# Kernel tuning notes

Measured on AMD Instinct MI355X. Metric: run time of the kernel, lower is better.

## Reference

```python
import jax, jax.numpy as jnp
import numpy as np

N_NODES = 100000


def gcn_conv(x, src, dst, W, b, n_nodes):
    # GCNConv: h = x @ W, then symmetric-normalized aggregation (self-loops already in src/dst)
    h = x @ W  # [N, out]
    ones = jnp.ones(src.shape[0], dtype=h.dtype)
    deg = jax.ops.segment_sum(ones, dst, num_segments=n_nodes)  # in-degree incl. self-loop
    dinv = jnp.where(deg > 0, jax.lax.rsqrt(deg), 0.0)
    norm = dinv[src] * dinv[dst]  # [E]
    msg = h[src] * norm[:, None]  # [E, out] gather
    out = jax.ops.segment_sum(msg, dst, num_segments=n_nodes)  # scatter-add
    return out + b


def setup_inputs() -> dict:
    key = jax.random.key(0)
    k1, k2, k3, k4 = jax.random.split(key, 4)
    n, f, h, c, e = N_NODES, 256, 128, 40, 1600000
    x = jax.random.normal(k1, (n, f), dtype=jnp.float32)
    edge_index = jax.random.randint(k2, (2, e), 0, n, dtype=jnp.int64)
    W1 = jax.random.normal(k3, (f, h), dtype=jnp.float32) * (1.0 / np.sqrt(f))
    b1 = jnp.zeros((h,), dtype=jnp.float32)
    W2 = jax.random.normal(k4, (h, c), dtype=jnp.float32) * (1.0 / np.sqrt(h))
    b2 = jnp.zeros((c,), dtype=jnp.float32)
    return {"x": x, "edge_index": edge_index, "W1": W1, "b1": b1, "W2": W2, "b2": b2}


def reference(x, edge_index, W1, b1, W2, b2):
    n = x.shape[0]
    loops = jnp.arange(n, dtype=edge_index.dtype)
    src = jnp.concatenate([edge_index[0], loops])
    dst = jnp.concatenate([edge_index[1], loops])
    h = jax.nn.relu(gcn_conv(x, src, dst, W1, b1, n))
    # dropout is identity in eval mode (self.training == False)
    logits = gcn_conv(h, src, dst, W2, b2, n)
    return jax.nn.log_softmax(logits, axis=1)
```

## Files before the change

### kernel.cpp

```cpp
#include <hip/hip_runtime.h>
#include <hip/hip_fp16.h>
#include <math.h>

#define FIN 256
#define HID 128
#define NCLS 40
#define ZPB 64
#define BKT_SHIFT 9
#define BKT_SZ 512
#define CHUNK 2048
#define CAP 12288

typedef __attribute__((ext_vector_type(8))) short short8_t;
typedef __attribute__((ext_vector_type(8))) _Float16 half8_t;
typedef __attribute__((ext_vector_type(4))) float f32x4;
typedef __attribute__((ext_vector_type(2))) float f32x2;

static __device__ __forceinline__ ushort f2bf(float f) {
    unsigned u = __float_as_uint(f);
    u += 0x7FFF + ((u >> 16) & 1);
    return (ushort)(u >> 16);
}

static __device__ __forceinline__ unsigned pack_ew(int s, float w) {
    return ((unsigned)s << 15) | (__float_as_uint(w) >> 17);
}


__global__ void k_prep(int* __restrict__ bcur, const float* __restrict__ W1,
                       ushort* __restrict__ Wt, const float* __restrict__ W2,
                       __half* __restrict__ W2t, int nbk) {
    int i = blockIdx.x * 256 + threadIdx.x;
    if (i <= nbk) bcur[i] = 0;
    if (i < FIN * HID) {
        int c = i >> 8, k = i & 255;
        Wt[i] = f2bf(W1[(size_t)k * HID + c]);
    }
    if (i < 48 * HID) {
        int c = i >> 7, k = i & 127;
        W2t[i] = __float2half((c < NCLS) ? W2[(size_t)k * NCLS + c] : 0.f);
    }
}


__global__ __launch_bounds__(256) void k_g1bkt(const float* __restrict__ X,
                                               const ushort* __restrict__ Wt,
                                               unsigned char* __restrict__ H8, int M,
                                               const int* __restrict__ src,
                                               const int* __restrict__ dst, int E,
                                               int* __restrict__ bcur,
                                               unsigned* __restrict__ ebkt,
                                               int nbk, int nbkb) {
    __shared__ uint4 wlds[128 * 32];
    int tid = threadIdx.x;

    if ((int)blockIdx.x < nbkb) {
        int* hist  = (int*)wlds;
        int* scanb = hist + 256;
        int* base  = scanb + 256;
        int* gbase = base + 256;
        unsigned* stage = (unsigned*)(gbase + 256);
        unsigned char* sbk = (unsigned char*)(stage + CHUNK);
        int e0 = blockIdx.x * CHUNK;
        int cntc = min(CHUNK, E - e0);
        hist[tid] = 0;
        __syncthreads();

        int s_[8], d_[8], bk_[8], rk_[8];
#pragma unroll
        for (int i = 0; i < 8; i++) {
            int j = tid + i * 256;
            if (j < cntc) {
                int s = src[e0 + j], d = dst[e0 + j];
                s_[i] = s; d_[i] = d;
                bk_[i] = d >> BKT_SHIFT;
                rk_[i] = atomicAdd(&hist[bk_[i]], 1);
            } else {
                bk_[i] = -1;
            }
        }
        __syncthreads();

        scanb[tid] = hist[tid];
        __syncthreads();
        for (int o = 1; o < 256; o <<= 1) {
            int u = (tid >= o) ? scanb[tid - o] : 0;
            __syncthreads();
            scanb[tid] += u;
            __syncthreads();
        }
        base[tid] = scanb[tid] - hist[tid];
        if (tid < nbk && hist[tid] > 0) gbase[tid] = atomicAdd(&bcur[tid], hist[tid]);
        __syncthreads();

#pragma unroll
        for (int i = 0; i < 8; i++) {
            if (bk_[i] >= 0) {
                int p = base[bk_[i]] + rk_[i];
                stage[p] = ((unsigned)s_[i] << 9) | ((unsigned)d_[i] & 511u);
                sbk[p] = (unsigned char)bk_[i];
            }
        }
        __syncthreads();

#pragma unroll
        for (int i = 0; i < 8; i++) {
            int j = tid + i * 256;
            if (j < cntc) {
                int bk = sbk[j];
                ebkt[(size_t)bk * CAP + gbase[bk] + (j - base[bk])] = stage[j];
            }
        }
        return;
    }

    int bid = blockIdx.x - nbkb;
    const uint4* wg = (const uint4*)Wt;
#pragma unroll
    for (int i = 0; i < 16; i++) {
        int e = tid + i * 256;
        int r = e >> 5, ch = e & 31;
        wlds[r * 32 + (ch ^ (r & 7))] = wg[e];
    }

    int wid = tid >> 6, lane = tid & 63;
    int q = lane & 15, kg = lane >> 4;
    int grow_in = bid * 64 + wid * 16 + q;
    int lrow = min(grow_in, M - 1);
    const float* xr = X + (size_t)lrow * FIN;

    float4 xf0[8], xf1[8];
#pragma unroll
    for (int kt = 0; kt < 8; kt++) {
        int k0 = kt * 32 + kg * 8;
        xf0[kt] = *(const float4*)(xr + k0);
        xf1[kt] = *(const float4*)(xr + k0 + 4);
    }
    __syncthreads();

    f32x4 acc[8];
#pragma unroll
    for (int c = 0; c < 8; c++) acc[c] = (f32x4){0.f, 0.f, 0.f, 0.f};

#pragma unroll
    for (int kt = 0; kt < 8; kt++) {
        unsigned r0, r1, r2, r3;
        asm("v_cvt_pk_bf16_f32 %0, %1, %2" : "=v"(r0) : "v"(xf0[kt].x), "v"(xf0[kt].y));
        asm("v_cvt_pk_bf16_f32 %0, %1, %2" : "=v"(r1) : "v"(xf0[kt].z), "v"(xf0[kt].w));
        asm("v_cvt_pk_bf16_f32 %0, %1, %2" : "=v"(r2) : "v"(xf1[kt].x), "v"(xf1[kt].y));
        asm("v_cvt_pk_bf16_f32 %0, %1, %2" : "=v"(r3) : "v"(xf1[kt].z), "v"(xf1[kt].w));
        union { uint4 u; short8_t s; } cv;
        cv.u = make_uint4(r0, r1, r2, r3);
        short8_t a = cv.s;
        int ch = kt * 4 + kg;
#pragma unroll
        for (int c = 0; c < 8; c++) {
            int col = c * 16 + q;
            short8_t b = *(const short8_t*)&wlds[col * 32 + (ch ^ (col & 7))];
            acc[c] = __builtin_amdgcn_mfma_f32_16x16x32_bf16(a, b, acc[c], 0, 0, 0);
        }
    }

    __syncthreads();
    float* st = (float*)wlds;
#pragma unroll
    for (int c = 0; c < 8; c++) {
        int col = c * 16 + q;
#pragma unroll
        for (int i = 0; i < 4; i++) {
            int lr = wid * 16 + kg * 4 + i;
            st[lr * 132 + col] = acc[c][i];
        }
    }
    __syncthreads();
    int orow = tid >> 2, seg = tid & 3;
    int grow = bid * 64 + orow;
    if (grow < M) {
        const float* sp = st + orow * 132 + seg * 32;
        unsigned u[8];
#pragma unroll
        for (int k = 0; k < 8; k++) {
            int p = 0;
            p = __builtin_amdgcn_cvt_pk_fp8_f32(sp[4 * k + 0], sp[4 * k + 1], p, false);
            p = __builtin_amdgcn_cvt_pk_fp8_f32(sp[4 * k + 2], sp[4 * k + 3], p, true);
            u[k] = (unsigned)p;
        }
        uint4* op = (uint4*)(H8 + (size_t)grow * HID + seg * 32);
        op[0] = make_uint4(u[0], u[1], u[2], u[3]);
        op[1] = make_uint4(u[4], u[5], u[6], u[7]);
    }
}


__global__ __launch_bounds__(512) void k_cnt(const unsigned* __restrict__ ebkt,
                                             int* __restrict__ bcur, int nbk,
                                             int* __restrict__ off, int* __restrict__ cnt,
                                             float* __restrict__ dinv, int n) {
    __shared__ int lcnt[BKT_SZ];
    __shared__ int lofs[BKT_SZ];
    __shared__ int lbase;
    int b = blockIdx.x, t = threadIdx.x;
    int n0 = b << BKT_SHIFT;
    lcnt[t] = 0;
    __syncthreads();
    int sz = bcur[b];
    const unsigned* ep = ebkt + (size_t)b * CAP;
    for (int e = t; e < sz; e += 512) atomicAdd(&lcnt[ep[e] & 511u], 1);
    __syncthreads();
    if (t == 0) lbase = atomicAdd(&bcur[nbk], sz);
    lofs[t] = lcnt[t];
    __syncthreads();
    for (int o = 1; o < 512; o <<= 1) {
        int u = (t >= o) ? lofs[t - o] : 0;
        __syncthreads();
        lofs[t] += u;
        __syncthreads();
    }
    int node = n0 + t;
    if (node < n) {
        int c = lcnt[t];
        off[node] = lbase + lofs[t] - c;
        cnt[node] = c;
        dinv[node] = rsqrtf((float)(c + 1));
    }
}


__global__ __launch_bounds__(512) void k_place(const unsigned* __restrict__ ebkt,
                                               const int* __restrict__ bcur,
                                               const int* __restrict__ off,
                                               const float* __restrict__ dinv,
                                               unsigned* __restrict__ eew, int n) {
    __shared__ int curx[BKT_SZ];
    __shared__ float ldin[BKT_SZ];
    int b = blockIdx.x, t = threadIdx.x;
    int n0 = b << BKT_SHIFT;
    int node = n0 + t;
    if (node < n) {
        curx[t] = off[node];
        ldin[t] = dinv[node];
    }
    __syncthreads();
    int sz = bcur[b];
    const unsigned* ep = ebkt + (size_t)b * CAP;
    for (int e = t; e < sz; e += 512) {
        unsigned ed = ep[e];
        int s = (int)(ed >> 9), dl = (int)(ed & 511u);
        float w = dinv[s] * ldin[dl];
        int pos = atomicAdd(&curx[dl], 1);
        eew[pos] = pack_ew(s, w);
    }
}


__global__ __launch_bounds__(256) void k_agg1(const unsigned char* __restrict__ H8,
                                              const unsigned* __restrict__ eew,
                                              const int* __restrict__ off,
                                              const int* __restrict__ cnt,
                                              const float* __restrict__ dinv,
                                              const float* __restrict__ b1,
                                              __half* __restrict__ H2, int n) {
    int tid = threadIdx.x;
    int node = blockIdx.x * 16 + (tid >> 4);
    int q = tid & 15;
    if (node >= n) return;
    float di = dinv[node];
    int start = off[node], ne = cnt[node];

    float acc[8];
    {
        uint2 v = *(const uint2*)(H8 + (size_t)node * HID + q * 8);
        float wv = di * di;
        f32x2 f;
        f = __builtin_amdgcn_cvt_pk_f32_fp8((int)v.x, false);
        acc[0] = f[0] * wv; acc[1] = f[1] * wv;
        f = __builtin_amdgcn_cvt_pk_f32_fp8((int)v.x, true);
        acc[2] = f[0] * wv; acc[3] = f[1] * wv;
        f = __builtin_amdgcn_cvt_pk_f32_fp8((int)v.y, false);
        acc[4] = f[0] * wv; acc[5] = f[1] * wv;
        f = __builtin_amdgcn_cvt_pk_f32_fp8((int)v.y, true);
        acc[6] = f[0] * wv; acc[7] = f[1] * wv;
    }

#pragma unroll 2
    for (int j = 0; j < ne; ++j) {
        unsigned u = eew[start + j];
        int s = (int)(u >> 15);
        float wv = __uint_as_float((u & 0x7FFFu) << 17);
        uint2 v = *(const uint2*)(H8 + (size_t)s * HID + q * 8);
        f32x2 f;
        f = __builtin_amdgcn_cvt_pk_f32_fp8((int)v.x, false);
        acc[0] = fmaf(f[0], wv, acc[0]); acc[1] = fmaf(f[1], wv, acc[1]);
        f = __builtin_amdgcn_cvt_pk_f32_fp8((int)v.x, true);
        acc[2] = fmaf(f[0], wv, acc[2]); acc[3] = fmaf(f[1], wv, acc[3]);
        f = __builtin_amdgcn_cvt_pk_f32_fp8((int)v.y, false);
        acc[4] = fmaf(f[0], wv, acc[4]); acc[5] = fmaf(f[1], wv, acc[5]);
        f = __builtin_amdgcn_cvt_pk_f32_fp8((int)v.y, true);
        acc[6] = fmaf(f[0], wv, acc[6]); acc[7] = fmaf(f[1], wv, acc[7]);
    }

    float r[8];
#pragma unroll
    for (int i = 0; i < 8; i++) r[i] = fmaxf(acc[i] + b1[q * 8 + i], 0.f);
    __half2 p0 = __floats2half2_rn(r[0], r[1]);
    __half2 p1 = __floats2half2_rn(r[2], r[3]);
    __half2 p2 = __floats2half2_rn(r[4], r[5]);
    __half2 p3 = __floats2half2_rn(r[6], r[7]);
    uint4 o4;
    o4.x = *(unsigned*)&p0; o4.y = *(unsigned*)&p1;
    o4.z = *(unsigned*)&p2; o4.w = *(unsigned*)&p3;
    *(uint4*)(H2 + (size_t)node * HID + q * 8) = o4;
}


__global__ __launch_bounds__(256) void k_gemm2(const __half* __restrict__ H2,
                                               const __half* __restrict__ W2t,
                                               unsigned char* __restrict__ Z8, int M) {
    int tid = threadIdx.x;
    int wid = tid >> 6, lane = tid & 63;
    int q = lane & 15, kg = lane >> 4;
    int row = blockIdx.x * 64 + wid * 16 + q;
    int lrow = min(row, M - 1);
    const __half* hr = H2 + (size_t)lrow * HID;

    half8_t a[4];
#pragma unroll
    for (int kt = 0; kt < 4; kt++) a[kt] = *(const half8_t*)(hr + kt * 32 + kg * 8);

    f32x4 acc[3];
#pragma unroll
    for (int c = 0; c < 3; c++) acc[c] = (f32x4){0.f, 0.f, 0.f, 0.f};

#pragma unroll
    for (int c = 0; c < 3; c++) {
        const __half* wc = W2t + (size_t)(c * 16 + q) * HID + kg * 8;
#pragma unroll
        for (int kt = 0; kt < 4; kt++) {
            half8_t b = *(const half8_t*)(wc + kt * 32);
            acc[c] = __builtin_amdgcn_mfma_f32_16x16x32_f16(a[kt], b, acc[c], 0, 0, 0);
        }
    }

    int r0 = blockIdx.x * 64 + wid * 16 + kg * 4;
#pragma unroll
    for (int c = 0; c < 3; c++) {
        int col = c * 16 + q;
        if (col < NCLS) {
#pragma unroll
            for (int i = 0; i < 4; i++) {
                int r = r0 + i;
                if (r < M) {
                    int p = __builtin_amdgcn_cvt_pk_fp8_f32(acc[c][i], acc[c][i], 0, false);
                    Z8[(size_t)r * ZPB + col] = (unsigned char)(p & 0xff);
                }
            }
        }
    }
}


__global__ __launch_bounds__(256) void k_agg2(const unsigned char* __restrict__ Z8,
                                              const unsigned* __restrict__ eew,
                                              const int* __restrict__ off,
                                              const int* __restrict__ cnt,
                                              const float* __restrict__ dinv,
                                              const float* __restrict__ b2,
                                              float* __restrict__ Out, int n) {
    int tid = threadIdx.x;
    int node = blockIdx.x * 32 + (tid >> 3);
    int l = tid & 7;
    if (node >= n) return;
    float di = dinv[node];
    int start = off[node], ne = cnt[node];

    float acc[8];
    {
        uint2 v = *(const uint2*)(Z8 + (size_t)node * ZPB + l * 8);
        float wv = di * di;
        f32x2 f;
        f = __builtin_amdgcn_cvt_pk_f32_fp8((int)v.x, false);
        acc[0] = f[0] * wv; acc[1] = f[1] * wv;
        f = __builtin_amdgcn_cvt_pk_f32_fp8((int)v.x, true);
        acc[2] = f[0] * wv; acc[3] = f[1] * wv;
        f = __builtin_amdgcn_cvt_pk_f32_fp8((int)v.y, false);
        acc[4] = f[0] * wv; acc[5] = f[1] * wv;
        f = __builtin_amdgcn_cvt_pk_f32_fp8((int)v.y, true);
        acc[6] = f[0] * wv; acc[7] = f[1] * wv;
    }

#pragma unroll 2
    for (int j = 0; j < ne; ++j) {
        unsigned u = eew[start + j];
        int s = (int)(u >> 15);
        float wv = __uint_as_float((u & 0x7FFFu) << 17);
        uint2 v = *(const uint2*)(Z8 + (size_t)s * ZPB + l * 8);
        f32x2 f;
        f = __builtin_amdgcn_cvt_pk_f32_fp8((int)v.x, false);
        acc[0] = fmaf(f[0], wv, acc[0]); acc[1] = fmaf(f[1], wv, acc[1]);
        f = __builtin_amdgcn_cvt_pk_f32_fp8((int)v.x, true);
        acc[2] = fmaf(f[0], wv, acc[2]); acc[3] = fmaf(f[1], wv, acc[3]);
        f = __builtin_amdgcn_cvt_pk_f32_fp8((int)v.y, false);
        acc[4] = fmaf(f[0], wv, acc[4]); acc[5] = fmaf(f[1], wv, acc[5]);
        f = __builtin_amdgcn_cvt_pk_f32_fp8((int)v.y, true);
        acc[6] = fmaf(f[0], wv, acc[6]); acc[7] = fmaf(f[1], wv, acc[7]);
    }

    bool valid = (l < 5);
    float v[8];
    float m = -INFINITY;
#pragma unroll
    for (int i = 0; i < 8; i++) {
        v[i] = valid ? acc[i] + b2[l * 8 + i] : -INFINITY;
        m = fmaxf(m, v[i]);
    }
#pragma unroll
    for (int o = 1; o <= 4; o <<= 1) m = fmaxf(m, __shfl_xor(m, o));
    float ssum = 0.f;
#pragma unroll
    for (int i = 0; i < 8; i++)
        if (valid) ssum += __expf(v[i] - m);
#pragma unroll
    for (int o = 1; o <= 4; o <<= 1) ssum += __shfl_xor(ssum, o);
    float lse = m + logf(ssum);

    if (valid) {
        float4 w0 = make_float4(v[0] - lse, v[1] - lse, v[2] - lse, v[3] - lse);
        float4 w1 = make_float4(v[4] - lse, v[5] - lse, v[6] - lse, v[7] - lse);
        float* op = Out + (size_t)node * NCLS + l * 8;
        *(float4*)op = w0;
        *(float4*)(op + 4) = w1;
    }
}


extern "C" void kernel_launch(void* const* d_in, const int* in_sizes, int n_in,
                              void* d_out, int out_size, void* d_ws, size_t ws_size,
                              hipStream_t stream) {
    const float* x  = (const float*)d_in[0];
    const int* ei   = (const int*)d_in[1];
    const float* W1 = (const float*)d_in[2];
    const float* b1 = (const float*)d_in[3];
    const float* W2 = (const float*)d_in[4];
    const float* b2 = (const float*)d_in[5];
    float* out = (float*)d_out;

    const int n = in_sizes[0] / FIN;
    const int E = in_sizes[1] / 2;
    const int* src = ei;
    const int* dst = ei + E;
    const int nbk = (n + BKT_SZ - 1) >> BKT_SHIFT;

    char* w = (char*)d_ws;
    auto alloc = [&](size_t bytes) {
        char* p = w;
        w += (bytes + 255) & ~(size_t)255;
        return p;
    };
    int* off     = (int*)alloc((size_t)n * 4);
    int* cnt     = (int*)alloc((size_t)n * 4);
    float* dinv  = (float*)alloc((size_t)n * 4);
    int* bcur    = (int*)alloc((size_t)(nbk + 1) * 4);
    unsigned* ebkt = (unsigned*)alloc((size_t)nbk * CAP * 4);
    unsigned* eew  = (unsigned*)alloc((size_t)E * 4);
    ushort* wt   = (ushort*)alloc((size_t)FIN * HID * 2);
    __half* w2t  = (__half*)alloc((size_t)48 * HID * 2);
    unsigned char* H8 = (unsigned char*)alloc((size_t)n * HID);
    __half* H2   = (__half*)alloc((size_t)n * HID * 2);
    unsigned char* Z8 = (unsigned char*)alloc((size_t)n * ZPB);

    const int nbkb = (E + CHUNK - 1) / CHUNK;
    const int g1b = (n + 63) / 64;

    k_prep<<<(FIN * HID) / 256, 256, 0, stream>>>(bcur, W1, wt, W2, w2t, nbk);

    k_g1bkt<<<nbkb + g1b, 256, 0, stream>>>(x, wt, H8, n, src, dst, E, bcur, ebkt, nbk, nbkb);

    k_cnt<<<nbk, 512, 0, stream>>>(ebkt, bcur, nbk, off, cnt, dinv, n);
    k_place<<<nbk, 512, 0, stream>>>(ebkt, bcur, off, dinv, eew, n);

    k_agg1<<<(n + 15) / 16, 256, 0, stream>>>(H8, eew, off, cnt, dinv, b1, H2, n);

    k_gemm2<<<(n + 63) / 64, 256, 0, stream>>>(H2, w2t, Z8, n);
    k_agg2<<<(n + 31) / 32, 256, 0, stream>>>(Z8, eew, off, cnt, dinv, b2, out, n);
}
```

Measured before the change: 163.8 us.

## Read W1 directly from global and store GEMM1 output in permuted column layout

The GEMM1 branch no longer stages W1 into shared memory. Each lane reads B fragments straight from global (L2/L1) and packs MFMA accumulators directly to fp8 without an LDS transpose, which removes two block barriers and the LDS round trip. H8 columns are therefore stored in a permuted order, and this is compensated by permuting W2's rows in prep and the b1 index in the aggregation. The cost is repeated global loads of W1 per block and narrower 8-byte scattered stores, and the shared footprint drops to just the bucketing arrays.

Measured after the change: 200.2 us. 1.22x slower.

```diff
diff --git a/kernel.cpp b/kernel.cpp
--- a/kernel.cpp
+++ b/kernel.cpp
@@ -27,6 +27,7 @@
 }
 
 
+
 __global__ void k_prep(int* __restrict__ bcur, const float* __restrict__ W1,
                        ushort* __restrict__ Wt, const float* __restrict__ W2,
                        __half* __restrict__ W2t, int nbk) {
@@ -37,7 +38,8 @@
         Wt[i] = f2bf(W1[(size_t)k * HID + c]);
     }
     if (i < 48 * HID) {
-        int c = i >> 7, k = i & 127;
+        int c = i >> 7, p = i & 127;
+        int k = (p & 7) * 16 + (p >> 3);
         W2t[i] = __float2half((c < NCLS) ? W2[(size_t)k * NCLS + c] : 0.f);
     }
 }
@@ -51,16 +53,15 @@
                                                int* __restrict__ bcur,
                                                unsigned* __restrict__ ebkt,
                                                int nbk, int nbkb) {
-    __shared__ uint4 wlds[128 * 32];
+    __shared__ int hist[256];
+    __shared__ int scanb[256];
+    __shared__ int base[256];
+    __shared__ int gbase[256];
+    __shared__ unsigned stage[CHUNK];
+    __shared__ unsigned char sbk[CHUNK];
     int tid = threadIdx.x;
 
     if ((int)blockIdx.x < nbkb) {
-        int* hist  = (int*)wlds;
-        int* scanb = hist + 256;
-        int* base  = scanb + 256;
-        int* gbase = base + 256;
-        unsigned* stage = (unsigned*)(gbase + 256);
-        unsigned char* sbk = (unsigned char*)(stage + CHUNK);
         int e0 = blockIdx.x * CHUNK;
         int cntc = min(CHUNK, E - e0);
         hist[tid] = 0;
@@ -115,14 +116,6 @@
     }
 
     int bid = blockIdx.x - nbkb;
-    const uint4* wg = (const uint4*)Wt;
-#pragma unroll
-    for (int i = 0; i < 16; i++) {
-        int e = tid + i * 256;
-        int r = e >> 5, ch = e & 31;
-        wlds[r * 32 + (ch ^ (r & 7))] = wg[e];
-    }
-
     int wid = tid >> 6, lane = tid & 63;
     int q = lane & 15, kg = lane >> 4;
     int grow_in = bid * 64 + wid * 16 + q;
@@ -136,7 +129,6 @@
         xf0[kt] = *(const float4*)(xr + k0);
         xf1[kt] = *(const float4*)(xr + k0 + 4);
     }
-    __syncthreads();
 
     f32x4 acc[8];
 #pragma unroll
@@ -152,42 +144,25 @@
         union { uint4 u; short8_t s; } cv;
         cv.u = make_uint4(r0, r1, r2, r3);
         short8_t a = cv.s;
-        int ch = kt * 4 + kg;
 #pragma unroll
         for (int c = 0; c < 8; c++) {
             int col = c * 16 + q;
-            short8_t b = *(const short8_t*)&wlds[col * 32 + (ch ^ (col & 7))];
+            short8_t b = *(const short8_t*)(Wt + (size_t)col * FIN + kt * 32 + kg * 8);
             acc[c] = __builtin_amdgcn_mfma_f32_16x16x32_bf16(a, b, acc[c], 0, 0, 0);
         }
     }
 
-    __syncthreads();
-    float* st = (float*)wlds;
-#pragma unroll
-    for (int c = 0; c < 8; c++) {
-        int col = c * 16 + q;
-#pragma unroll
-        for (int i = 0; i < 4; i++) {
-            int lr = wid * 16 + kg * 4 + i;
-            st[lr * 132 + col] = acc[c][i];
-        }
-    }
-    __syncthreads();
-    int orow = tid >> 2, seg = tid & 3;
-    int grow = bid * 64 + orow;
-    if (grow < M) {
-        const float* sp = st + orow * 132 + seg * 32;
-        unsigned u[8];
-#pragma unroll
-        for (int k = 0; k < 8; k++) {
-            int p = 0;
-            p = __builtin_amdgcn_cvt_pk_fp8_f32(sp[4 * k + 0], sp[4 * k + 1], p, false);
-            p = __builtin_amdgcn_cvt_pk_fp8_f32(sp[4 * k + 2], sp[4 * k + 3], p, true);
-            u[k] = (unsigned)p;
-        }
-        uint4* op = (uint4*)(H8 + (size_t)grow * HID + seg * 32);
-        op[0] = make_uint4(u[0], u[1], u[2], u[3]);
-        op[1] = make_uint4(u[4], u[5], u[6], u[7]);
+#pragma unroll
+    for (int i = 0; i < 4; i++) {
+        int r = bid * 64 + wid * 16 + kg * 4 + i;
+        if (r < M) {
+            int lo = 0, hi = 0;
+            lo = __builtin_amdgcn_cvt_pk_fp8_f32(acc[0][i], acc[1][i], lo, false);
+            lo = __builtin_amdgcn_cvt_pk_fp8_f32(acc[2][i], acc[3][i], lo, true);
+            hi = __builtin_amdgcn_cvt_pk_fp8_f32(acc[4][i], acc[5][i], hi, false);
+            hi = __builtin_amdgcn_cvt_pk_fp8_f32(acc[6][i], acc[7][i], hi, true);
+            *(uint2*)(H8 + (size_t)r * HID + q * 8) = make_uint2((unsigned)lo, (unsigned)hi);
+        }
     }
 }
 
@@ -301,7 +276,7 @@
 
     float r[8];
 #pragma unroll
-    for (int i = 0; i < 8; i++) r[i] = fmaxf(acc[i] + b1[q * 8 + i], 0.f);
+    for (int i = 0; i < 8; i++) r[i] = fmaxf(acc[i] + b1[i * 16 + q], 0.f);
     __half2 p0 = __floats2half2_rn(r[0], r[1]);
     __half2 p1 = __floats2half2_rn(r[2], r[3]);
     __half2 p2 = __floats2half2_rn(r[4], r[5]);
```
